# Optimization experiments

Measured on AMD Instinct MI355X. Metric: run time of the kernel, lower is better.

The kernel has to match this reference:

```python
import jax, jax.numpy as jnp
import numpy as np

D_MODEL = 1024
NUM_HEADS = 16
D_K = D_MODEL // NUM_HEADS
SCALE = float(np.sqrt(D_K))


def setup_inputs() -> dict:
    key = jax.random.key(0)
    ks = jax.random.split(key, 11)
    B, S, D = 2, 2048, D_MODEL
    def lin(kw):
        # xavier-uniform-ish weight, zero bias (matches torch init style)
        lim = float(np.sqrt(6.0 / (D + D)))
        return jax.random.uniform(kw, (D, D), jnp.float32, -lim, lim)
    return {
        "q": jax.random.normal(ks[0], (B, S, D), jnp.float32),
        "k": jax.random.normal(ks[1], (B, S, D), jnp.float32),
        "v": jax.random.normal(ks[2], (B, S, D), jnp.float32),
        "Wq": lin(ks[3]), "bq": jnp.zeros((D,), jnp.float32),
        "Wk": lin(ks[4]), "bk": jnp.zeros((D,), jnp.float32),
        "Wv": lin(ks[5]), "bv": jnp.zeros((D,), jnp.float32),
        "Wo": lin(ks[6]), "bo": jnp.zeros((D,), jnp.float32),
    }


def _split_heads(x):
    B, S, _ = x.shape
    return x.reshape(B, S, NUM_HEADS, D_K).transpose(0, 2, 1, 3)  # (B,H,S,dk)


def reference(q, k, v, Wq, bq, Wk, bk, Wv, bv, Wo, bo):
    # torch nn.Linear: y = x @ W.T + b
    Q = _split_heads(q @ Wq.T + bq)
    K = _split_heads(k @ Wk.T + bk)
    V = _split_heads(v @ Wv.T + bv)
    scores = jnp.einsum("bhqd,bhkd->bhqk", Q, K) / SCALE
    # numerically-stable softmax with detached max (as in the torch code)
    m = jax.lax.stop_gradient(jnp.max(scores, axis=-1, keepdims=True))
    exp_scores = jnp.exp(scores - m)
    attn = exp_scores / (jnp.sum(exp_scores, axis=-1, keepdims=True) + 1e-9)
    out = jnp.einsum("bhqk,bhkd->bhqd", attn, V)  # (B,H,S,dk)
    B, H, S, dk = out.shape
    out = out.transpose(0, 2, 1, 3).reshape(B, S, H * dk)
    return out @ Wo.T + bo
```

## Files before the change

### kernel.cpp

```cpp
#include <hip/hip_runtime.h>


#define D_MODEL 1024
#define NHEADS  16
#define DKH     64
#define SEQ     2048
#define BATCH   2
#define MTOT    (BATCH * SEQ)
#define XE      ((long)MTOT * D_MODEL)
#define WE      ((long)D_MODEL * D_MODEL)
#define QSCALE  0.18033688011112042f

typedef __attribute__((ext_vector_type(8)))  short short8v;
typedef __attribute__((ext_vector_type(4)))  short short4v;
typedef __attribute__((ext_vector_type(4)))  float f32x4;
typedef __attribute__((ext_vector_type(16))) float f32x16;

typedef __attribute__((address_space(1))) void as1_void;
typedef __attribute__((address_space(3))) void as3_void;

__device__ __forceinline__ void gload16(const void* g, void* l) {
    __builtin_amdgcn_global_load_lds((const as1_void*)g, (as3_void*)l, 16, 0, 0);
}

__device__ __forceinline__ unsigned short f2bf(float x) {
    unsigned int u = __float_as_uint(x);
    u += 0x7FFFu + ((u >> 16) & 1u);
    return (unsigned short)(u >> 16);
}

__device__ __forceinline__ float fexp2(float x) {
    return __builtin_amdgcn_exp2f(x);
}

__device__ __forceinline__ unsigned int cvt_pk_bf16(float lo, float hi) {
    unsigned int r;
    asm("v_cvt_pk_bf16_f32 %0, %1, %2" : "=v"(r) : "v"(lo), "v"(hi));
    return r;
}

__device__ __forceinline__ int swz_u(int row, int col) {
    int byte = (col << 1) ^ ((row & 7) << 4);
    return (row << 6) + (byte >> 1);
}

__device__ __forceinline__ int swz_v(int d, int kv) {
    int slot = (d & 6) | ((d >> 3) & 1);
    int byte = (kv << 1) ^ (slot << 4);
    return (d << 6) + (byte >> 1);
}

struct ConvArgs {
    const float*    src[7];
    unsigned short* dst[7];
    int             n4[7];
};

__global__ __launch_bounds__(256) void convert_kernel(ConvArgs a) {
    int z = blockIdx.y;
    const float4*   s = (const float4*)a.src[z];
    unsigned short* d = a.dst[z];
    int n = a.n4[z];
    for (int i = blockIdx.x * blockDim.x + threadIdx.x; i < n;
         i += gridDim.x * blockDim.x) {
        float4 v = s[i];
        ushort4 o;
        o.x = f2bf(v.x); o.y = f2bf(v.y); o.z = f2bf(v.z); o.w = f2bf(v.w);
        *(ushort4*)(d + 4L * i) = o;
    }
}

__device__ __forceinline__ void stv(float* p, float v)          { *p = v; }
__device__ __forceinline__ void stv(unsigned short* p, float v) { *p = f2bf(v); }

template <typename OutT>
__device__ __forceinline__ void gemm_core(const unsigned short* __restrict__ A,
                                          const unsigned short* __restrict__ Bm,
                                          const float* __restrict__ bias,
                                          OutT* __restrict__ C,
                                          int K, int N, float scale) {
    __shared__ unsigned short As[128 * 32];
    __shared__ unsigned short Bs[128 * 32];

    const int t    = threadIdx.x;
    const int lane = t & 63;
    const int w    = t >> 6;
    const int wm   = w >> 1, wn = w & 1;
    const int l15  = lane & 15, g = lane >> 4;
    const long m0  = (long)blockIdx.y * 128;
    const long n0  = (long)blockIdx.x * 128;

    f32x4 acc[4][4] = {};

    const int idx0 = t, idx1 = t + 256;
    const int r0 = idx0 >> 2, c0 = (idx0 & 3) * 8;
    const int r1 = idx1 >> 2, c1 = (idx1 & 3) * 8;
    const unsigned short* pa0 = A  + (m0 + r0) * K + c0;
    const unsigned short* pa1 = A  + (m0 + r1) * K + c1;
    const unsigned short* pb0 = Bm + (n0 + r0) * K + c0;
    const unsigned short* pb1 = Bm + (n0 + r1) * K + c1;

    for (int k0 = 0; k0 < K; k0 += 32) {
        gload16(pa0 + k0, &As[idx0 * 8]);
        gload16(pa1 + k0, &As[idx1 * 8]);
        gload16(pb0 + k0, &Bs[idx0 * 8]);
        gload16(pb1 + k0, &Bs[idx1 * 8]);
        __syncthreads();

        short8v af[4], bf_[4];
#pragma unroll
        for (int mf = 0; mf < 4; ++mf)
            af[mf] = *(const short8v*)&As[(wm * 64 + mf * 16 + l15) * 32 + g * 8];
#pragma unroll
        for (int nf = 0; nf < 4; ++nf)
            bf_[nf] = *(const short8v*)&Bs[(wn * 64 + nf * 16 + l15) * 32 + g * 8];
#pragma unroll
        for (int mf = 0; mf < 4; ++mf)
#pragma unroll
            for (int nf = 0; nf < 4; ++nf)
                acc[mf][nf] = __builtin_amdgcn_mfma_f32_16x16x32_bf16(
                    af[mf], bf_[nf], acc[mf][nf], 0, 0, 0);
        __syncthreads();
    }

    float bvv[4];
#pragma unroll
    for (int nf = 0; nf < 4; ++nf)
        bvv[nf] = bias[n0 + wn * 64 + nf * 16 + l15];

#pragma unroll
    for (int mf = 0; mf < 4; ++mf)
#pragma unroll
        for (int nf = 0; nf < 4; ++nf)
#pragma unroll
            for (int r = 0; r < 4; ++r) {
                long row = m0 + wm * 64 + mf * 16 + g * 4 + r;
                long col = n0 + wn * 64 + nf * 16 + l15;
                float v = (acc[mf][nf][r] + bvv[nf]) * scale;
                stv(C + row * (long)N + col, v);
            }
}

__global__ __launch_bounds__(256) void proj_kernel(
    const unsigned short* __restrict__ xb, const unsigned short* __restrict__ wb,
    const float* __restrict__ bq, const float* __restrict__ bk,
    const float* __restrict__ bv, unsigned short* __restrict__ qkv) {
    int z = blockIdx.z;
    const float* bias = (z == 0) ? bq : (z == 1) ? bk : bv;
    float scale = (z == 0) ? QSCALE : 1.0f;
    gemm_core<unsigned short>(xb + (long)z * XE, wb + (long)z * WE, bias,
                              qkv + (long)z * XE, D_MODEL, D_MODEL, scale);
}

__global__ __launch_bounds__(256) void out_kernel(
    const unsigned short* __restrict__ ob, const unsigned short* __restrict__ wo,
    const float* __restrict__ bo, float* __restrict__ out) {
    gemm_core<float>(ob, wo, bo, out, D_MODEL, D_MODEL, 1.0f);
}

#define TSZ 4096
#define NTS 16

__global__ __launch_bounds__(512) void attn_kernel(
    const unsigned short* __restrict__ Qb, const unsigned short* __restrict__ Kb,
    const unsigned short* __restrict__ Vb, unsigned short* __restrict__ Ob) {
    __shared__ alignas(16) unsigned char SM[69120];
    unsigned short* KsB   = (unsigned short*)SM;
    unsigned short* VtB   = (unsigned short*)(SM + 32768);
    float*          corrS = (float*)(SM + 65536);
    float*          mS    = (float*)(SM + 66560);
    float*          lS    = (float*)(SM + 67584);
    float*          lTot  = (float*)(SM + 68608);
    float*          comb  = (float*)SM;

    const int t = threadIdx.x, lane = t & 63, w = t >> 6;
    const int l31 = lane & 31, h = lane >> 5;
    const int qg = w & 3, sp = w >> 2;
    const int bh = blockIdx.y;
    const long headoff = (long)(bh >> 4) * SEQ * D_MODEL + (long)(bh & 15) * DKH;
    const int q0w = blockIdx.x * 128 + qg * 32;

    short8v qf[4];
#pragma unroll
    for (int step = 0; step < 4; ++step)
        qf[step] = *(const short8v*)(Qb + headoff +
            (long)(q0w + l31) * D_MODEL + step * 16 + h * 8);

    f32x16 o[2] = {};
    float mrun = -3.0e38f;
    float lrun = 0.f;

    const int vtile = t >> 8, t8 = t & 255;
    const int vd0  = (t8 & 31) * 2;
    const int vkv0 = (t8 >> 5) * 8;
    const int kr0 = t >> 3, ks0 = t & 7;

    unsigned int va[8];

#define ISSUE_V(kt)                                                        \
    _Pragma("unroll")                                                      \
    for (int j = 0; j < 8; ++j)                                            \
        va[j] = *(const unsigned int*)(Vb + headoff +                      \
            (long)((kt) + vtile * 64 + vkv0 + j) * D_MODEL + vd0);

#define ISSUE_K(kt, dbuf)                                                  \
    gload16(Kb + headoff + (long)((kt) + kr0) * D_MODEL +                  \
                ((ks0 ^ (kr0 & 7)) << 3),                                  \
            &KsB[((dbuf) * 2 + 0) * TSZ + t * 8]);                         \
    gload16(Kb + headoff + (long)((kt) + 64 + kr0) * D_MODEL +             \
                ((ks0 ^ (kr0 & 7)) << 3),                                  \
            &KsB[((dbuf) * 2 + 1) * TSZ + t * 8]);

#define WRITE_V(dbuf)                                                      \
    {                                                                      \
        short8v ra, rb;                                                    \
        _Pragma("unroll")                                                  \
        for (int j = 0; j < 8; ++j) {                                      \
            ra[j] = (short)(va[j] & 0xffffu);                              \
            rb[j] = (short)(va[j] >> 16);                                  \
        }                                                                  \
        unsigned short* vt = &VtB[((dbuf) * 2 + vtile) * TSZ];             \
        *(short8v*)&vt[swz_v(vd0,     vkv0)] = ra;                         \
        *(short8v*)&vt[swz_v(vd0 + 1, vkv0)] = rb;                         \
    }

    asm volatile("s_waitcnt vmcnt(0)" ::: "memory");
    ISSUE_V(0);
    ISSUE_K(0, 0);
    WRITE_V(0);
    int cur = 0;

    for (int it = 0; it < NTS; ++it) {
        const int nxt = cur ^ 1;
        const int ktn = ((it + 1) & (NTS - 1)) * 128;
        ISSUE_V(ktn);
        ISSUE_K(ktn, nxt);
        asm volatile("s_waitcnt vmcnt(10)" ::: "memory");
        asm volatile("s_waitcnt lgkmcnt(0)" ::: "memory");
        __builtin_amdgcn_sched_barrier(0);
        __builtin_amdgcn_s_barrier();
        __builtin_amdgcn_sched_barrier(0);

        const int kO = (cur * 2 + sp) * TSZ;

        f32x16 st[2] = {};
        __builtin_amdgcn_s_setprio(1);
#pragma unroll
        for (int step = 0; step < 4; ++step) {
            short8v kf0 = *(const short8v*)&KsB[kO + swz_u(l31,      step * 16 + h * 8)];
            st[0] = __builtin_amdgcn_mfma_f32_32x32x16_bf16(kf0, qf[step], st[0], 0, 0, 0);
            short8v kf1 = *(const short8v*)&KsB[kO + swz_u(32 + l31, step * 16 + h * 8)];
            st[1] = __builtin_amdgcn_mfma_f32_32x32x16_bf16(kf1, qf[step], st[1], 0, 0, 0);
        }
        __builtin_amdgcn_s_setprio(0);

        float m01[8];
#pragma unroll
        for (int j = 0; j < 8; ++j)
            m01[j] = fmaxf(fmaxf(st[0][2 * j], st[0][2 * j + 1]),
                           fmaxf(st[1][2 * j], st[1][2 * j + 1]));
        float vmax = fmaxf(fmaxf(fmaxf(fmaxf(m01[0], m01[1]), m01[2]),
                                 fmaxf(fmaxf(m01[3], m01[4]), m01[5])),
                           fmaxf(m01[6], m01[7]));
        vmax = fmaxf(vmax, __shfl_xor(vmax, 32));

        const bool grow = __any(vmax > mrun + 8.0f);
        if (grow) {
            float mnew = fmaxf(mrun, vmax);
            float corr = fexp2(mrun - mnew);
            mrun = mnew;
            lrun *= corr;
            if (lane < 32) corrS[w * 32 + l31] = corr;
#pragma unroll
            for (int q2 = 0; q2 < 4; ++q2) {
                float4 cv = *(const float4*)&corrS[w * 32 + q2 * 8 + h * 4];
#pragma unroll
                for (int r3 = 0; r3 < 4; ++r3) {
                    o[0][q2 * 4 + r3] *= cv[r3];
                    o[1][q2 * 4 + r3] *= cv[r3];
                }
            }
        }

        float ps = 0.f;
#pragma unroll
        for (int b = 0; b < 2; ++b)
#pragma unroll
            for (int r = 0; r < 16; ++r) {
                st[b][r] = fexp2(st[b][r] - mrun);
                ps += st[b][r];
            }
        ps += __shfl_xor(ps, 32);
        lrun += ps;

        __builtin_amdgcn_s_setprio(1);
#pragma unroll
        for (int b = 0; b < 2; ++b)
#pragma unroll
            for (int s = 0; s < 2; ++s) {
                unsigned int u  = cvt_pk_bf16(st[b][s * 8 + 0], st[b][s * 8 + 1]);
                unsigned int u2 = cvt_pk_bf16(st[b][s * 8 + 2], st[b][s * 8 + 3]);
                unsigned int v  = cvt_pk_bf16(st[b][s * 8 + 4], st[b][s * 8 + 5]);
                unsigned int v2 = cvt_pk_bf16(st[b][s * 8 + 6], st[b][s * 8 + 7]);
                asm("v_permlane32_swap_b32 %0, %1" : "+v"(u),  "+v"(v));
                asm("v_permlane32_swap_b32 %0, %1" : "+v"(u2), "+v"(v2));
                uint4 pu = {u, u2, v, v2};
                short8v pa = __builtin_bit_cast(short8v, pu);
                short8v vb0 = *(const short8v*)&VtB[kO + swz_v(l31,      b * 32 + s * 16 + h * 8)];
                o[0] = __builtin_amdgcn_mfma_f32_32x32x16_bf16(pa, vb0, o[0], 0, 0, 0);
                short8v vb1 = *(const short8v*)&VtB[kO + swz_v(32 + l31, b * 32 + s * 16 + h * 8)];
                o[1] = __builtin_amdgcn_mfma_f32_32x32x16_bf16(pa, vb1, o[1], 0, 0, 0);
            }
        __builtin_amdgcn_s_setprio(0);

        WRITE_V(nxt);
        cur = nxt;
    }

    asm volatile("s_waitcnt vmcnt(0)" ::: "memory");

    if (lane < 32) {
        mS[(sp * 4 + qg) * 32 + l31] = mrun;
        lS[(sp * 4 + qg) * 32 + l31] = lrun;
    }
    __syncthreads();

#pragma unroll
    for (int q2 = 0; q2 < 4; ++q2) {
        float4 ma = *(const float4*)&mS[(0 * 4 + qg) * 32 + q2 * 8 + h * 4];
        float4 mb = *(const float4*)&mS[(1 * 4 + qg) * 32 + q2 * 8 + h * 4];
#pragma unroll
        for (int r3 = 0; r3 < 4; ++r3) {
            float mt = fmaxf(ma[r3], mb[r3]);
            float mo = (sp == 0) ? ma[r3] : mb[r3];
            float sc = fexp2(mo - mt);
            o[0][q2 * 4 + r3] *= sc;
            o[1][q2 * 4 + r3] *= sc;
        }
    }

    if (sp == 1) {
#pragma unroll
        for (int c = 0; c < 16; ++c) {
            comb[(c)        * 256 + qg * 64 + lane] = o[0][c];
            comb[(c + 16)   * 256 + qg * 64 + lane] = o[1][c];
        }
    }
    __syncthreads();
    if (sp == 0) {
#pragma unroll
        for (int c = 0; c < 16; ++c) {
            o[0][c] += comb[(c)      * 256 + qg * 64 + lane];
            o[1][c] += comb[(c + 16) * 256 + qg * 64 + lane];
        }
        float m0 = mS[(0 * 4 + qg) * 32 + l31];
        float m1 = mS[(1 * 4 + qg) * 32 + l31];
        float mt = fmaxf(m0, m1);
        float lt = lS[(0 * 4 + qg) * 32 + l31] * fexp2(m0 - mt) +
                   lS[(1 * 4 + qg) * 32 + l31] * fexp2(m1 - mt);
        if (lane < 32) lTot[qg * 32 + l31] = lt;
#pragma unroll
        for (int q2 = 0; q2 < 4; ++q2)
#pragma unroll
            for (int r3 = 0; r3 < 4; ++r3) {
                float inv = 1.f / (lTot[qg * 32 + q2 * 8 + h * 4 + r3] + 1e-9f);
                long rowoff = headoff +
                    (long)(q0w + q2 * 8 + h * 4 + r3) * D_MODEL;
                Ob[rowoff + l31]      = f2bf(o[0][q2 * 4 + r3] * inv);
                Ob[rowoff + 32 + l31] = f2bf(o[1][q2 * 4 + r3] * inv);
            }
    }
#undef ISSUE_V
#undef ISSUE_K
#undef WRITE_V
}

extern "C" void kernel_launch(void* const* d_in, const int* in_sizes, int n_in,
                              void* d_out, int out_size, void* d_ws, size_t ws_size,
                              hipStream_t stream) {
    unsigned short* ws  = (unsigned short*)d_ws;
    unsigned short* xb  = ws;
    unsigned short* wb  = ws + 3L * XE;
    unsigned short* qkv = ws + 3L * XE + 4L * WE;
    unsigned short* ob  = qkv + 3L * XE;

    ConvArgs ca;
    ca.src[0] = (const float*)d_in[0]; ca.dst[0] = xb;           ca.n4[0] = (int)(XE / 4);
    ca.src[1] = (const float*)d_in[1]; ca.dst[1] = xb + XE;      ca.n4[1] = (int)(XE / 4);
    ca.src[2] = (const float*)d_in[2]; ca.dst[2] = xb + 2L * XE; ca.n4[2] = (int)(XE / 4);
    ca.src[3] = (const float*)d_in[3]; ca.dst[3] = wb;           ca.n4[3] = (int)(WE / 4);
    ca.src[4] = (const float*)d_in[5]; ca.dst[4] = wb + WE;      ca.n4[4] = (int)(WE / 4);
    ca.src[5] = (const float*)d_in[7]; ca.dst[5] = wb + 2L * WE; ca.n4[5] = (int)(WE / 4);
    ca.src[6] = (const float*)d_in[9]; ca.dst[6] = wb + 3L * WE; ca.n4[6] = (int)(WE / 4);

    hipLaunchKernelGGL(convert_kernel, dim3(512, 7), dim3(256), 0, stream, ca);

    hipLaunchKernelGGL(proj_kernel, dim3(8, 32, 3), dim3(256), 0, stream,
                       xb, wb, (const float*)d_in[4], (const float*)d_in[6],
                       (const float*)d_in[8], qkv);

    hipLaunchKernelGGL(attn_kernel, dim3(16, 32), dim3(512), 0, stream,
                       qkv, qkv + XE, qkv + 2L * XE, ob);

    hipLaunchKernelGGL(out_kernel, dim3(8, 32), dim3(256), 0, stream,
                       ob, wb + 3L * WE, (const float*)d_in[10], (float*)d_out);
}
```

Before: 142.2 us.

## Remap blocks to XCDs for L2 locality and single-buffer V tile

```diff
diff --git a/kernel.cpp b/kernel.cpp
--- a/kernel.cpp
+++ b/kernel.cpp
@@ -78,7 +78,8 @@
                                           const unsigned short* __restrict__ Bm,
                                           const float* __restrict__ bias,
                                           OutT* __restrict__ C,
-                                          int K, int N, float scale) {
+                                          int K, int N, float scale,
+                                          long m0, long n0) {
     __shared__ unsigned short As[128 * 32];
     __shared__ unsigned short Bs[128 * 32];
 
@@ -87,8 +88,6 @@
     const int w    = t >> 6;
     const int wm   = w >> 1, wn = w & 1;
     const int l15  = lane & 15, g = lane >> 4;
-    const long m0  = (long)blockIdx.y * 128;
-    const long n0  = (long)blockIdx.x * 128;
 
     f32x4 acc[4][4] = {};
 
@@ -145,17 +144,29 @@
     const unsigned short* __restrict__ xb, const unsigned short* __restrict__ wb,
     const float* __restrict__ bq, const float* __restrict__ bk,
     const float* __restrict__ bv, unsigned short* __restrict__ qkv) {
-    int z = blockIdx.z;
+    const int bid = blockIdx.x;
+    const int xcd = bid & 7;
+    const int k   = bid >> 3;
+    const int ty  = (xcd << 2) | (k & 3);
+    const int tx  = (k >> 2) & 7;
+    const int z   = k >> 5;
     const float* bias = (z == 0) ? bq : (z == 1) ? bk : bv;
     float scale = (z == 0) ? QSCALE : 1.0f;
     gemm_core<unsigned short>(xb + (long)z * XE, wb + (long)z * WE, bias,
-                              qkv + (long)z * XE, D_MODEL, D_MODEL, scale);
+                              qkv + (long)z * XE, D_MODEL, D_MODEL, scale,
+                              (long)ty * 128, (long)tx * 128);
 }
 
 __global__ __launch_bounds__(256) void out_kernel(
     const unsigned short* __restrict__ ob, const unsigned short* __restrict__ wo,
     const float* __restrict__ bo, float* __restrict__ out) {
-    gemm_core<float>(ob, wo, bo, out, D_MODEL, D_MODEL, 1.0f);
+    const int bid = blockIdx.x;
+    const int xcd = bid & 7;
+    const int k   = bid >> 3;
+    const int ty  = (xcd << 2) | (k & 3);
+    const int tx  = k >> 2;
+    gemm_core<float>(ob, wo, bo, out, D_MODEL, D_MODEL, 1.0f,
+                     (long)ty * 128, (long)tx * 128);
 }
 
 #define TSZ 4096
@@ -164,21 +175,25 @@
 __global__ __launch_bounds__(512) void attn_kernel(
     const unsigned short* __restrict__ Qb, const unsigned short* __restrict__ Kb,
     const unsigned short* __restrict__ Vb, unsigned short* __restrict__ Ob) {
-    __shared__ alignas(16) unsigned char SM[69120];
+    __shared__ alignas(16) unsigned char SM[52736];
     unsigned short* KsB   = (unsigned short*)SM;
     unsigned short* VtB   = (unsigned short*)(SM + 32768);
-    float*          corrS = (float*)(SM + 65536);
-    float*          mS    = (float*)(SM + 66560);
-    float*          lS    = (float*)(SM + 67584);
-    float*          lTot  = (float*)(SM + 68608);
+    float*          corrS = (float*)(SM + 49152);
+    float*          mS    = (float*)(SM + 50176);
+    float*          lS    = (float*)(SM + 51200);
+    float*          lTot  = (float*)(SM + 52224);
     float*          comb  = (float*)SM;
 
     const int t = threadIdx.x, lane = t & 63, w = t >> 6;
     const int l31 = lane & 31, h = lane >> 5;
     const int qg = w & 3, sp = w >> 2;
-    const int bh = blockIdx.y;
+    const int bid = blockIdx.x;
+    const int xcd = bid & 7;
+    const int kk2 = bid >> 3;
+    const int bh  = (xcd << 2) | (kk2 & 3);
+    const int qb  = kk2 >> 2;
     const long headoff = (long)(bh >> 4) * SEQ * D_MODEL + (long)(bh & 15) * DKH;
-    const int q0w = blockIdx.x * 128 + qg * 32;
+    const int q0w = qb * 128 + qg * 32;
 
     short8v qf[4];
 #pragma unroll
@@ -211,7 +226,7 @@
                 ((ks0 ^ (kr0 & 7)) << 3),                                  \
             &KsB[((dbuf) * 2 + 1) * TSZ + t * 8]);
 
-#define WRITE_V(dbuf)                                                      \
+#define WRITE_V()                                                          \
     {                                                                      \
         short8v ra, rb;                                                    \
         _Pragma("unroll")                                                  \
@@ -219,7 +234,7 @@
             ra[j] = (short)(va[j] & 0xffffu);                              \
             rb[j] = (short)(va[j] >> 16);                                  \
         }                                                                  \
-        unsigned short* vt = &VtB[((dbuf) * 2 + vtile) * TSZ];             \
+        unsigned short* vt = &VtB[vtile * TSZ];                            \
         *(short8v*)&vt[swz_v(vd0,     vkv0)] = ra;                         \
         *(short8v*)&vt[swz_v(vd0 + 1, vkv0)] = rb;                         \
     }
@@ -227,7 +242,7 @@
     asm volatile("s_waitcnt vmcnt(0)" ::: "memory");
     ISSUE_V(0);
     ISSUE_K(0, 0);
-    WRITE_V(0);
+    WRITE_V();
     int cur = 0;
 
     for (int it = 0; it < NTS; ++it) {
@@ -242,6 +257,7 @@
         __builtin_amdgcn_sched_barrier(0);
 
         const int kO = (cur * 2 + sp) * TSZ;
+        const int vO = sp * TSZ;
 
         f32x16 st[2] = {};
         __builtin_amdgcn_s_setprio(1);
@@ -306,14 +322,17 @@
                 asm("v_permlane32_swap_b32 %0, %1" : "+v"(u2), "+v"(v2));
                 uint4 pu = {u, u2, v, v2};
                 short8v pa = __builtin_bit_cast(short8v, pu);
-                short8v vb0 = *(const short8v*)&VtB[kO + swz_v(l31,      b * 32 + s * 16 + h * 8)];
+                short8v vb0 = *(const short8v*)&VtB[vO + swz_v(l31,      b * 32 + s * 16 + h * 8)];
                 o[0] = __builtin_amdgcn_mfma_f32_32x32x16_bf16(pa, vb0, o[0], 0, 0, 0);
-                short8v vb1 = *(const short8v*)&VtB[kO + swz_v(32 + l31, b * 32 + s * 16 + h * 8)];
+                short8v vb1 = *(const short8v*)&VtB[vO + swz_v(32 + l31, b * 32 + s * 16 + h * 8)];
                 o[1] = __builtin_amdgcn_mfma_f32_32x32x16_bf16(pa, vb1, o[1], 0, 0, 0);
             }
         __builtin_amdgcn_s_setprio(0);
 
-        WRITE_V(nxt);
+        __builtin_amdgcn_sched_barrier(0);
+        __builtin_amdgcn_s_barrier();
+        __builtin_amdgcn_sched_barrier(0);
+        WRITE_V();
         cur = nxt;
     }
 
@@ -395,13 +414,13 @@
 
     hipLaunchKernelGGL(convert_kernel, dim3(512, 7), dim3(256), 0, stream, ca);
 
-    hipLaunchKernelGGL(proj_kernel, dim3(8, 32, 3), dim3(256), 0, stream,
+    hipLaunchKernelGGL(proj_kernel, dim3(768), dim3(256), 0, stream,
                        xb, wb, (const float*)d_in[4], (const float*)d_in[6],
                        (const float*)d_in[8], qkv);
 
-    hipLaunchKernelGGL(attn_kernel, dim3(16, 32), dim3(512), 0, stream,
+    hipLaunchKernelGGL(attn_kernel, dim3(512), dim3(512), 0, stream,
                        qkv, qkv + XE, qkv + 2L * XE, ob);
 
-    hipLaunchKernelGGL(out_kernel, dim3(8, 32), dim3(256), 0, stream,
+    hipLaunchKernelGGL(out_kernel, dim3(256), dim3(256), 0, stream,
                        ob, wb + 3L * WE, (const float*)d_in[10], (float*)d_out);
 }
```

Result: faster. 137.9 us (-3.0%).
